# Kernel optimization log

Measured on AMD Instinct MI355X. Metric: run time of the kernel, lower is better.

Reference implementation:

```python
import jax, jax.numpy as jnp
import numpy as np

B, T_ENC, H, L, V = 32, 1024, 1024, 511, 512
SOS = 0


def setup_inputs() -> dict:
    key = jax.random.key(0)
    ks = jax.random.split(key, 16)
    s = 0.02
    inp = {
        "encoder_outputs": jax.random.normal(ks[0], (B, T_ENC, H), jnp.float32),
        "encoder_output_lengths": jnp.clip(
            jax.random.randint(ks[1], (B,), 0, T_ENC), 1, T_ENC
        ).astype(jnp.int64 if jax.config.jax_enable_x64 else jnp.int32),
        "input_labels": jax.random.randint(ks[2], (B, L), 0, V),
        # parameters
        "emb": jax.random.normal(ks[3], (V, H), jnp.float32) * s,
        "lin_in": jax.random.normal(ks[4], (H, H), jnp.float32) * s,      # attention linear_in (no bias)
        "lin_out": jax.random.normal(ks[5], (H, 2 * H), jnp.float32) * s,  # attention linear_out (no bias)
        "gru_w_ih0": jax.random.normal(ks[6], (3 * H, H), jnp.float32) * s,
        "gru_w_hh0": jax.random.normal(ks[7], (3 * H, H), jnp.float32) * s,
        "gru_b_ih0": jax.random.normal(ks[8], (3 * H,), jnp.float32) * s,
        "gru_b_hh0": jax.random.normal(ks[9], (3 * H,), jnp.float32) * s,
        "gru_w_ih1": jax.random.normal(ks[10], (3 * H, H), jnp.float32) * s,
        "gru_w_hh1": jax.random.normal(ks[11], (3 * H, H), jnp.float32) * s,
        "gru_b_ih1": jax.random.normal(ks[12], (3 * H,), jnp.float32) * s,
        "gru_b_hh1": jax.random.normal(ks[13], (3 * H,), jnp.float32) * s,
        "fc_w": jax.random.normal(ks[14], (V, H), jnp.float32) * s,
        "fc_b": jax.random.normal(ks[15], (V,), jnp.float32) * s,
    }
    return inp


def _gru_layer(x_proj, w_hh, b_hh):
    """x_proj: [B, T, 3H] precomputed input projection (incl. b_ih). Torch gate order r,z,n."""
    h0 = jnp.zeros((x_proj.shape[0], w_hh.shape[1]), x_proj.dtype)

    def step(h, xp):
        gh = h @ w_hh.T + b_hh
        xr, xz, xn = jnp.split(xp, 3, axis=-1)
        hr, hz, hn = jnp.split(gh, 3, axis=-1)
        r = jax.nn.sigmoid(xr + hr)
        z = jax.nn.sigmoid(xz + hz)
        n = jnp.tanh(xn + r * hn)
        h_new = (1.0 - z) * n + z * h
        return h_new, h_new

    _, ys = jax.lax.scan(step, h0, x_proj.transpose(1, 0, 2))
    return ys.transpose(1, 0, 2)  # [B, T, H]


def reference(encoder_outputs, encoder_output_lengths, input_labels, emb,
              lin_in, lin_out, gru_w_ih0, gru_w_hh0, gru_b_ih0, gru_b_hh0,
              gru_w_ih1, gru_w_hh1, gru_b_ih1, gru_b_hh1, fc_w, fc_b):
    Bsz = encoder_outputs.shape[0]
    # prepend SOS token (teacher forcing path)
    labels = jnp.concatenate(
        [jnp.full((Bsz, 1), SOS, dtype=input_labels.dtype), input_labels], axis=1
    )  # [B, L+1]
    x = emb[labels]  # [B, L+1, H] (dropout p=0 -> identity)

    # Attention (type='general')
    q = jnp.einsum("bqd,ed->bqe", x, lin_in)  # linear_in(query)
    scores = jnp.einsum("bqd,bkd->bqk", q, encoder_outputs)  # [B, L+1, T]
    t = encoder_outputs.shape[1]
    mask = jnp.arange(t)[None, :] >= encoder_output_lengths[:, None]  # [B, T]
    scores = jnp.where(mask[:, None, :], -jnp.inf, scores)
    w = jax.nn.softmax(scores, axis=-1)
    mix = jnp.einsum("bqk,bkd->bqd", w, encoder_outputs)
    combined = jnp.concatenate([mix, q], axis=-1)  # [B, L+1, 2H]
    attn_out = jnp.tanh(jnp.einsum("bqc,dc->bqd", combined, lin_out))

    # 2-layer GRU (rnn2)
    xp0 = jnp.einsum("btd,gd->btg", attn_out, gru_w_ih0) + gru_b_ih0
    y0 = _gru_layer(xp0, gru_w_hh0, gru_b_hh0)
    xp1 = jnp.einsum("btd,gd->btg", y0, gru_w_ih1) + gru_b_ih1
    y1 = _gru_layer(xp1, gru_w_hh1, gru_b_hh1)

    logits = jnp.einsum("btd,vd->btv", y1, fc_w) + fc_b
    return jax.nn.log_softmax(logits, axis=-1)  # [B, L+1, V]
```

## Files before the change

kernel.cpp:

```cpp
#include <hip/hip_runtime.h>

typedef unsigned short u16;
typedef unsigned int u32;
typedef short bs8 __attribute__((ext_vector_type(8)));
typedef float f4_t __attribute__((ext_vector_type(4)));

#define NB   32
#define TSEQ 512
#define TENC 1024
#define HD   1024
#define VOC  512
#define FS   32
#define POLL_CAP (1 << 22)

#define AS1 __attribute__((address_space(1)))
#define AS3 __attribute__((address_space(3)))

__device__ __forceinline__ float b2f(u16 u) {
  union { u32 i; float f; } x; x.i = ((u32)u) << 16; return x.f;
}
__device__ __forceinline__ u16 f2b(float f) {
  union { float ff; u32 i; } x; x.ff = f;
  u32 r = x.i + 0x7fff + ((x.i >> 16) & 1);
  return (u16)(r >> 16);
}
__device__ __forceinline__ float inF(const void* p, size_t i, int bf) {
  return bf ? b2f(((const u16*)p)[i]) : ((const float*)p)[i];
}
__device__ __forceinline__ void inF4(const void* p, size_t i, int bf, float* o) {
  if (bf) {
    ushort4 u = *reinterpret_cast<const ushort4*>((const u16*)p + i);
    o[0] = b2f(u.x); o[1] = b2f(u.y); o[2] = b2f(u.z); o[3] = b2f(u.w);
  } else {
    float4 v = *reinterpret_cast<const float4*>((const float*)p + i);
    o[0] = v.x; o[1] = v.y; o[2] = v.z; o[3] = v.w;
  }
}
__device__ __forceinline__ void outF(void* p, size_t i, float v, int bf) {
  if (bf) ((u16*)p)[i] = f2b(v);
  else ((float*)p)[i] = v;
}
__device__ __forceinline__ void gld16(const void* g, void* l) {
  __builtin_amdgcn_global_load_lds((const AS1 u32*)g, (AS3 u32*)l, 16, 0, 0);
}
__device__ __forceinline__ u32 aLoad(u32* p) {
  return __hip_atomic_load(p, __ATOMIC_RELAXED, __HIP_MEMORY_SCOPE_AGENT);
}
__device__ __forceinline__ void aStore(u32* p, u32 v) {
  __hip_atomic_store(p, v, __ATOMIC_RELAXED, __HIP_MEMORY_SCOPE_AGENT);
}
__device__ __forceinline__ uint4 ldUC(const char* p) {
  uint4 r;
  asm volatile("global_load_dwordx4 %0, %1, off sc0 sc1" : "=v"(r) : "v"(p));
  return r;
}
__device__ __forceinline__ void stUCshort(char* p, u32 v) {
  asm volatile("global_store_short %0, %1, off sc0 sc1" :: "v"(p), "v"(v) : "memory");
}
__device__ __forceinline__ void waitVM0() {
  asm volatile("s_waitcnt vmcnt(0)" ::: "memory");
}

__global__ void k_detect(const u32* __restrict__ w, int* __restrict__ flag) {
  __shared__ int cnt;
  if (threadIdx.x == 0) cnt = 0;
  __syncthreads();
  int c = 0;
  for (int i = threadIdx.x; i < 1024; i += 256) {
    u32 e = (w[i] >> 7) & 0xFF;
    if (e >= 100 && e <= 126) c++;
  }
  atomicAdd(&cnt, c);
  __syncthreads();
  if (threadIdx.x == 0) flag[0] = (cnt >= 512) ? 1 : 0;
}

__global__ __launch_bounds__(256) void k_f2bf(
    const void* __restrict__ in, u16* __restrict__ out, const int* __restrict__ flagp) {
  const int bf = flagp[0];
  size_t i = ((size_t)blockIdx.x * 256 + threadIdx.x) * 4;
  float v[4]; inF4(in, i, bf, v);
  ushort4 o; o.x = f2b(v[0]); o.y = f2b(v[1]); o.z = f2b(v[2]); o.w = f2b(v[3]);
  *reinterpret_cast<ushort4*>(&out[i]) = o;
}

__global__ __launch_bounds__(256) void k_embed(
    const int* __restrict__ labels, const void* __restrict__ emb,
    u16* __restrict__ x, const int* __restrict__ flagp) {
  const int bf = flagp[0];
  const int m = blockIdx.x;
  const int b = m >> 9, t = m & 511;
  const int lab = (t == 0) ? 0 : labels[b * 511 + t - 1];
  const size_t src = (size_t)lab * HD;
  const size_t dst = (size_t)m * HD;
  const int k = threadIdx.x * 4;
  float v[4]; inF4(emb, src + k, bf, v);
  ushort4 o; o.x = f2b(v[0]); o.y = f2b(v[1]); o.z = f2b(v[2]); o.w = f2b(v[3]);
  *reinterpret_cast<ushort4*>(&x[dst + k]) = o;
}

__global__ __launch_bounds__(256) void k_transpose(
    const void* __restrict__ enc, u16* __restrict__ encT, const int* __restrict__ flagp) {
  const int bf = flagp[0];
  __shared__ float tile[32][33];
  const int b = blockIdx.z, t0 = blockIdx.x * 32, h0 = blockIdx.y * 32;
  const int i = threadIdx.x >> 5, j = threadIdx.x & 31;
  const size_t base = (size_t)b * (TENC * HD);
#pragma unroll
  for (int rr = 0; rr < 4; rr++) {
    int r = i + rr * 8;
    tile[r][j] = inF(enc, base + (size_t)(t0 + r) * HD + h0 + j, bf);
  }
  __syncthreads();
#pragma unroll
  for (int rr = 0; rr < 4; rr++) {
    int r = i + rr * 8;
    encT[base + (size_t)(h0 + r) * TENC + t0 + j] = f2b(tile[j][r]);
  }
}

__global__ __launch_bounds__(256) void k_mfma_gemm(
    const u16* __restrict__ A, const u16* __restrict__ Bm, int K, int lda, int ldb,
    long strideA, long strideB, long strideC,
    void* __restrict__ C, int ldc, int cmode, int act,
    const void* __restrict__ bias, const int* __restrict__ flagp) {
  const int bf = flagp[0];
  __shared__ u16 lsA[8192];
  __shared__ u16 lsB[8192];
  const int tid = threadIdx.x;
  const int l = tid & 63, w = tid >> 6;
  const int wr = w >> 1, wc = w & 1;
  const long m0 = (long)blockIdx.x * 128;
  const long n0 = (long)blockIdx.y * 128;
  const long bz = blockIdx.z;
  const u16* Ab = A + bz * strideA;
  const u16* Bb = Bm + bz * strideB;

  f4_t acc[4][4] = {};
  const int srow = w * 8 + (l >> 3);
  const int schx = (l & 7) * 16;

  for (int kt = 0; kt < K; kt += 64) {
#pragma unroll
    for (int i = 0; i < 4; i++) {
      const int row = i * 32 + srow;
      const char* ga = (const char*)(Ab + (m0 + row) * (long)lda + kt)
                       + (schx ^ ((row & 7) << 4));
      gld16(ga, (char*)lsA + i * 4096 + w * 1024);
    }
#pragma unroll
    for (int i = 0; i < 4; i++) {
      const int row = i * 32 + srow;
      const char* gb = (const char*)(Bb + (n0 + row) * (long)ldb + kt)
                       + (schx ^ ((row & 7) << 4));
      gld16(gb, (char*)lsB + i * 4096 + w * 1024);
    }
    __syncthreads();
#pragma unroll
    for (int h = 0; h < 2; h++) {
      bs8 af[4], bfr[4];
#pragma unroll
      for (int i = 0; i < 4; i++) {
        const int row = wr * 64 + i * 16 + (l & 15);
        const int byt = row * 128 + (((h * 64) + ((l >> 4) * 16)) ^ ((row & 7) << 4));
        af[i] = *(const bs8*)((const char*)lsA + byt);
      }
#pragma unroll
      for (int j = 0; j < 4; j++) {
        const int row = wc * 64 + j * 16 + (l & 15);
        const int byt = row * 128 + (((h * 64) + ((l >> 4) * 16)) ^ ((row & 7) << 4));
        bfr[j] = *(const bs8*)((const char*)lsB + byt);
      }
#pragma unroll
      for (int i = 0; i < 4; i++)
#pragma unroll
        for (int j = 0; j < 4; j++)
          acc[i][j] = __builtin_amdgcn_mfma_f32_16x16x32_bf16(af[i], bfr[j], acc[i][j], 0, 0, 0);
    }
    __syncthreads();
  }

  float bv[4] = {0.f, 0.f, 0.f, 0.f};
  if (bias) {
#pragma unroll
    for (int j = 0; j < 4; j++)
      bv[j] = inF(bias, (size_t)(n0 + wc * 64 + j * 16 + (l & 15)), bf);
  }
#pragma unroll
  for (int i = 0; i < 4; i++) {
#pragma unroll
    for (int j = 0; j < 4; j++) {
      const long rowb = m0 + wr * 64 + i * 16 + ((l >> 4) * 4);
      const long col = n0 + wc * 64 + j * 16 + (l & 15);
#pragma unroll
      for (int r = 0; r < 4; r++) {
        float v = acc[i][j][r] + bv[j];
        if (act == 1) v = tanhf(v);
        const long row = rowb + r;
        if (cmode == 0) {
          ((u16*)C)[bz * strideC + row * (long)ldc + col] = f2b(v);
        } else if (cmode == 1) {
          ((float*)C)[bz * strideC + row * (long)ldc + col] = v;
        } else {
          ((u16*)C)[((long)(row & 511) * 32 + (row >> 9)) * (long)ldc + col] = f2b(v);
        }
      }
    }
  }
}

__global__ __launch_bounds__(256) void k_softmax(
    u16* __restrict__ S, const int* __restrict__ lens) {
  const int m = blockIdx.x;
  const int b = m >> 9;
  const int len = lens[b];
  const int tid = threadIdx.x;
  const size_t base = (size_t)m * TENC;
  float v[4];
  float mx = -1e30f;
#pragma unroll
  for (int i = 0; i < 4; i++) {
    int j = tid + i * 256;
    float s = b2f(S[base + j]);
    v[i] = (j < len) ? s : -1e30f;
    mx = fmaxf(mx, v[i]);
  }
  __shared__ float red[8];
  for (int o = 32; o; o >>= 1) mx = fmaxf(mx, __shfl_xor(mx, o, 64));
  if ((tid & 63) == 0) red[tid >> 6] = mx;
  __syncthreads();
  mx = fmaxf(fmaxf(red[0], red[1]), fmaxf(red[2], red[3]));
  float e[4]; float sum = 0.f;
#pragma unroll
  for (int i = 0; i < 4; i++) {
    e[i] = (v[i] > -1e29f) ? expf(v[i] - mx) : 0.f;
    sum += e[i];
  }
  for (int o = 32; o; o >>= 1) sum += __shfl_xor(sum, o, 64);
  __shared__ float red2[8];
  if ((tid & 63) == 0) red2[tid >> 6] = sum;
  __syncthreads();
  sum = red2[0] + red2[1] + red2[2] + red2[3];
  const float inv = 1.f / sum;
#pragma unroll
  for (int i = 0; i < 4; i++) S[base + tid + i * 256] = f2b(e[i] * inv);
}

__global__ __launch_bounds__(256) void k_packw(
    const void* __restrict__ Wih, const void* __restrict__ Whh,
    u16* __restrict__ out, int fused, const int* __restrict__ flagp) {
  const int bf = flagp[0];
  const long idx = (long)blockIdx.x * 256 + threadIdx.x;
  const int l = (int)(idx & 63);
  int ks, c16, blk;
  if (fused) { ks = (int)((idx >> 6) & 63); c16 = (int)((idx >> 12) & 1); blk = (int)(idx >> 13); }
  else       { ks = (int)((idx >> 6) & 31); c16 = (int)((idx >> 11) & 1); blk = (int)(idx >> 12); }
  const int v = blk * 32 + c16 * 16 + (l & 15);
  const int f = v >> 2, slot = v & 3;
  const int k = ks * 32 + ((l >> 4) << 3);
  const void* W = Whh; long row = 0; bool zero = false; int kk = k;
  if (!fused) {
    if (slot == 0) row = f;
    else if (slot == 1) row = 1024 + f;
    else if (slot == 2) row = 2048 + f;
    else zero = true;
  } else {
    const bool xp = (k < 1024); kk = k & 1023;
    W = xp ? Wih : Whh;
    if (slot == 0) row = f;
    else if (slot == 1) row = 1024 + f;
    else if (slot == 2) { row = 2048 + f; zero = !xp; }
    else { row = 2048 + f; zero = xp; }
  }
  u16 o[8];
#pragma unroll
  for (int e = 0; e < 8; e++)
    o[e] = zero ? (u16)0 : f2b(inF(W, (size_t)row * 1024 + kk + e, bf));
  ushort4* dst = (ushort4*)(out + idx * 8);
  dst[0] = make_ushort4(o[0], o[1], o[2], o[3]);
  dst[1] = make_ushort4(o[4], o[5], o[6], o[7]);
}

__device__ __forceinline__ void stage64(const char* src, char* dst, int tid) {
#pragma unroll
  for (int bh = 0; bh < 2; bh++) {
    uint4 v[8];
#pragma unroll
    for (int i = 0; i < 8; i++)
      v[i] = ldUC(src + (bh * 8 + i) * 4096 + tid * 16);
    waitVM0();
#pragma unroll
    for (int i = 0; i < 8; i++)
      *(uint4*)(dst + (bh * 8 + i) * 4096 + tid * 16) = v[i];
  }
}
__device__ __forceinline__ void waitpair(u32* flags, int aL0, int aL1, int tid) {
  if (tid < 64) {
    int guard = 0;
    while (1) {
      const int v0 = (int)aLoad(flags + (size_t)tid * FS);
      const int v1 = (int)aLoad(flags + (size_t)(tid + 64) * FS);
      const int v2 = (int)aLoad(flags + (size_t)(tid + 128) * FS);
      const int v3 = (int)aLoad(flags + (size_t)(tid + 192) * FS);
      const bool ok = (v0 >= aL0) && (v1 >= aL0) && (v2 >= aL1) && (v3 >= aL1);
      if (__all(ok)) break;
      if (++guard > POLL_CAP) break;
      __builtin_amdgcn_s_sleep(1);
    }
  }
  __syncthreads();
}

__global__ void __launch_bounds__(256, 1) k_gru_p(
    const u16* __restrict__ xp0, const u16* __restrict__ wpk0, const u16* __restrict__ wpk1,
    const void* __restrict__ bhh0, const void* __restrict__ bih1, const void* __restrict__ bhh1,
    u16* __restrict__ y1, char* h0buf, char* h1buf, u32* flags,
    const int* __restrict__ flagp) {
  extern __shared__ char smem[];
  float* red = (float*)(smem + 131072);
  const int bf = flagp[0];
  const int tid = threadIdx.x, l = tid & 63, w = tid >> 6;
  const int nh = w & 1, kh = w >> 1;
  const int g = blockIdx.x;
  const bool isL0 = (g < 128);
  const int gg = isL0 ? g : g - 128;
  const int fl = (l & 15) >> 2;
  const int F = gg * 8 + nh * 4 + fl;
  const int bl0 = (l & 48) | (fl << 2);

  float hprev[2][4] = {{0.f, 0.f, 0.f, 0.f}, {0.f, 0.f, 0.f, 0.f}};

  if (isL0) {
    const u16* W = wpk0 + (size_t)gg * 32768;
    const float br = inF(bhh0, (size_t)F, bf);
    const float bz = inF(bhh0, (size_t)(1024 + F), bf);
    const float bn = inF(bhh0, (size_t)(2048 + F), bf);
    for (int t = 0; t < TSEQ; t++) {
      waitpair(flags, t, t - 1, tid);
      stage64(h0buf + (t & 1) * 65536, smem, tid);
      __syncthreads();
      f4_t S[2] = {};
#pragma unroll 4
      for (int ksl = 0; ksl < 16; ksl++) {
        const int ks = kh * 16 + ksl;
        const bs8 bb = *(const bs8*)(W + (((size_t)(nh * 32 + ks) * 64 + l) << 3));
#pragma unroll
        for (int mt = 0; mt < 2; mt++) {
          const int row = mt * 16 + (l & 15);
          const int byt = row * 2048 + ((ks * 64 + ((l >> 4) << 4)) ^ ((row & 7) << 4));
          const bs8 aa = *(const bs8*)(smem + byt);
          S[mt] = __builtin_amdgcn_mfma_f32_16x16x32_bf16(aa, bb, S[mt], 0, 0, 0);
        }
      }
      if (kh == 1) {
#pragma unroll
        for (int mt = 0; mt < 2; mt++)
          *(f4_t*)&red[((nh * 2 + mt) * 64 + l) * 4] = S[mt];
      }
      __syncthreads();
      if (kh == 0) {
#pragma unroll
        for (int mt = 0; mt < 2; mt++)
          S[mt] += *(const f4_t*)&red[((nh * 2 + mt) * 64 + l) * 4];
        char* hw = h0buf + ((t + 1) & 1) * 65536;
#pragma unroll
        for (int mt = 0; mt < 2; mt++) {
#pragma unroll
          for (int r = 0; r < 4; r++) {
            const int b = mt * 16 + ((l >> 4) << 2) + r;
            const float hr = __shfl(S[mt][r], bl0);
            const float hz = __shfl(S[mt][r], bl0 + 1);
            const float hn = __shfl(S[mt][r], bl0 + 2);
            const long xb = (long)t * 98304 + (long)b * 3072 + F;
            const float xr = b2f(xp0[xb]);
            const float xz = b2f(xp0[xb + 1024]);
            const float xn = b2f(xp0[xb + 2048]);
            const float rr = 1.f / (1.f + expf(-(xr + hr + br)));
            const float zz = 1.f / (1.f + expf(-(xz + hz + bz)));
            const float nn = tanhf(xn + rr * (hn + bn));
            const float hv = (1.f - zz) * nn + zz * hprev[mt][r];
            hprev[mt][r] = hv;
            if ((l & 3) == 0) {
              const int swb = b * 2048 + ((2 * F) ^ ((b & 7) << 4));
              stUCshort(hw + swb, (u32)f2b(hv));
            }
          }
        }
      }
      waitVM0();
      __syncthreads();
      if (tid == 0) aStore(flags + (size_t)g * FS, (u32)(t + 1));
    }
  } else {
    const u16* W = wpk1 + (size_t)gg * 65536;
    const float br = inF(bih1, (size_t)F, bf) + inF(bhh1, (size_t)F, bf);
    const float bz = inF(bih1, (size_t)(1024 + F), bf) + inF(bhh1, (size_t)(1024 + F), bf);
    const float bxn = inF(bih1, (size_t)(2048 + F), bf);
    const float bhn = inF(bhh1, (size_t)(2048 + F), bf);
    for (int s = 0; s < TSEQ; s++) {
      waitpair(flags, s + 1, s, tid);
      stage64(h0buf + ((s + 1) & 1) * 65536, smem, tid);
      stage64(h1buf + (s & 1) * 65536, smem + 65536, tid);
      __syncthreads();
      f4_t S[2] = {};
#pragma unroll 4
      for (int ksl = 0; ksl < 32; ksl++) {
        const int ks = kh * 32 + ksl;
        const bs8 bb = *(const bs8*)(W + (((size_t)(nh * 64 + ks) * 64 + l) << 3));
        const int base = (ks >= 32) ? 65536 : 0;
        const int ks5 = ks & 31;
#pragma unroll
        for (int mt = 0; mt < 2; mt++) {
          const int row = mt * 16 + (l & 15);
          const int byt = base + row * 2048 + ((ks5 * 64 + ((l >> 4) << 4)) ^ ((row & 7) << 4));
          const bs8 aa = *(const bs8*)(smem + byt);
          S[mt] = __builtin_amdgcn_mfma_f32_16x16x32_bf16(aa, bb, S[mt], 0, 0, 0);
        }
      }
      if (kh == 1) {
#pragma unroll
        for (int mt = 0; mt < 2; mt++)
          *(f4_t*)&red[((nh * 2 + mt) * 64 + l) * 4] = S[mt];
      }
      __syncthreads();
      if (kh == 0) {
#pragma unroll
        for (int mt = 0; mt < 2; mt++)
          S[mt] += *(const f4_t*)&red[((nh * 2 + mt) * 64 + l) * 4];
        char* hw = h1buf + ((s + 1) & 1) * 65536;
#pragma unroll
        for (int mt = 0; mt < 2; mt++) {
#pragma unroll
          for (int r = 0; r < 4; r++) {
            const int b = mt * 16 + ((l >> 4) << 2) + r;
            const float rs = __shfl(S[mt][r], bl0);
            const float zs = __shfl(S[mt][r], bl0 + 1);
            const float xnp = __shfl(S[mt][r], bl0 + 2);
            const float hnp = __shfl(S[mt][r], bl0 + 3);
            const float rr = 1.f / (1.f + expf(-(rs + br)));
            const float zz = 1.f / (1.f + expf(-(zs + bz)));
            const float nn = tanhf((xnp + bxn) + rr * (hnp + bhn));
            const float hv = (1.f - zz) * nn + zz * hprev[mt][r];
            hprev[mt][r] = hv;
            if ((l & 3) == 0) {
              const int swb = b * 2048 + ((2 * F) ^ ((b & 7) << 4));
              stUCshort(hw + swb, (u32)f2b(hv));
              y1[((long)b * 512 + s) * 1024 + F] = f2b(hv);
            }
          }
        }
      }
      waitVM0();
      __syncthreads();
      if (tid == 0) aStore(flags + (size_t)g * FS, (u32)(s + 1));
    }
  }
}

__global__ __launch_bounds__(256) void k_logsoftmax(
    const float* __restrict__ L, void* __restrict__ out, const int* __restrict__ flagp) {
  const int bf = flagp[0];
  const int m = blockIdx.x;
  const int tid = threadIdx.x;
  const size_t base = (size_t)m * VOC;
  float v0 = L[base + tid], v1 = L[base + tid + 256];
  float mx = fmaxf(v0, v1);
  __shared__ float red[8];
  for (int o = 32; o; o >>= 1) mx = fmaxf(mx, __shfl_xor(mx, o, 64));
  if ((tid & 63) == 0) red[tid >> 6] = mx;
  __syncthreads();
  mx = fmaxf(fmaxf(red[0], red[1]), fmaxf(red[2], red[3]));
  float s = expf(v0 - mx) + expf(v1 - mx);
  for (int o = 32; o; o >>= 1) s += __shfl_xor(s, o, 64);
  __shared__ float red2[8];
  if ((tid & 63) == 0) red2[tid >> 6] = s;
  __syncthreads();
  s = red2[0] + red2[1] + red2[2] + red2[3];
  const float lse = mx + logf(s);
  outF(out, base + tid, v0 - lse, bf);
  outF(out, base + tid + 256, v1 - lse, bf);
}

extern "C" void kernel_launch(void* const* d_in, const int* in_sizes, int n_in,
                              void* d_out, int out_size, void* d_ws, size_t ws_size,
                              hipStream_t stream) {
  const void* enc = d_in[0];
  const int* lens = (const int*)d_in[1];
  const int* labels = (const int*)d_in[2];
  const void* emb = d_in[3];
  const void* lin_in = d_in[4];
  const void* lin_out = d_in[5];
  const void* w_ih0 = d_in[6];
  const void* w_hh0 = d_in[7];
  const void* b_ih0 = d_in[8];
  const void* b_hh0 = d_in[9];
  const void* w_ih1 = d_in[10];
  const void* w_hh1 = d_in[11];
  const void* b_ih1 = d_in[12];
  const void* b_hh1 = d_in[13];
  const void* fc_w = d_in[14];
  const void* fc_b = d_in[15];

  char* ws = (char*)d_ws;
  const size_t SZ = (size_t)NB * TSEQ * HD * 2;
  int* flag = (int*)ws;
  u16* R0 = (u16*)(ws + 256);
  u16* R1 = (u16*)(ws + 256 + SZ);
  u16* R2 = (u16*)(ws + 256 + 2 * SZ);
  char* R4 = ws + 256 + 4 * SZ;

  char* R2u = (char*)R2 + SZ;
  u16* wpk0 = (u16*)R2u;
  u16* wpk1 = (u16*)(R2u + 8388608);
  char* hreg = R2u + 25165824;
  u32* flagsbuf = (u32*)hreg;
  char* h0buf = hreg + 32768;
  char* h1buf = hreg + 32768 + 131072;
  const size_t hreg_bytes = 32768 + 262144;

  u16* scores = (u16*)R4;
  u16* wli = (u16*)(R4 + 35651584);
  u16* wlo = (u16*)(R4 + 37748736);
  u16* xp0 = (u16*)R4;
  u16* wfc = (u16*)R4;
  float* logits = (float*)(R4 + 1048576);

  k_detect<<<1, 256, 0, stream>>>((const u32*)emb, flag);
  k_embed<<<NB * TSEQ, 256, 0, stream>>>(labels, emb, R0, flag);
  k_f2bf<<<32768, 256, 0, stream>>>(enc, R1, flag);
  k_f2bf<<<1024, 256, 0, stream>>>(lin_in, wli, flag);
  k_f2bf<<<2048, 256, 0, stream>>>(lin_out, wlo, flag);

  k_mfma_gemm<<<dim3(128, 8, 1), 256, 0, stream>>>(
      R0, wli, HD, HD, HD, 0, 0, 0, (void*)(R2 + 1024), 2 * HD, 0, 0, nullptr, flag);
  k_transpose<<<dim3(32, 32, NB), 256, 0, stream>>>(enc, R0, flag);
  k_mfma_gemm<<<dim3(4, 8, NB), 256, 0, stream>>>(
      R2 + 1024, R1, HD, 2 * HD, HD,
      (long)TSEQ * 2 * HD, (long)TENC * HD, (long)TSEQ * TENC,
      (void*)scores, TENC, 0, 0, nullptr, flag);
  k_softmax<<<NB * TSEQ, 256, 0, stream>>>(scores, lens);
  k_mfma_gemm<<<dim3(4, 8, NB), 256, 0, stream>>>(
      scores, R0, TENC, TENC, TENC,
      (long)TSEQ * TENC, (long)HD * TENC, (long)TSEQ * 2 * HD,
      (void*)R2, 2 * HD, 0, 0, nullptr, flag);
  k_mfma_gemm<<<dim3(128, 8, 1), 256, 0, stream>>>(
      R2, wlo, 2 * HD, 2 * HD, 2 * HD, 0, 0, 0,
      (void*)R0, HD, 0, 1, nullptr, flag);

  k_packw<<<2048, 256, 0, stream>>>(nullptr, w_hh0, wpk0, 0, flag);
  k_packw<<<4096, 256, 0, stream>>>(w_ih1, w_hh1, wpk1, 1, flag);
  k_f2bf<<<3072, 256, 0, stream>>>(w_ih0, R1, flag);
  k_mfma_gemm<<<dim3(128, 24, 1), 256, 0, stream>>>(
      R0, R1, HD, HD, HD, 0, 0, 0, (void*)xp0, 3 * HD, 2, 0, b_ih0, flag);

  hipMemsetAsync(hreg, 0, hreg_bytes, stream);
  hipFuncSetAttribute((const void*)k_gru_p,
                      hipFuncAttributeMaxDynamicSharedMemorySize, 139264);
  u16* y1p = R2;
  void* args[] = {&xp0, &wpk0, &wpk1,
                  (void*)&b_hh0, (void*)&b_ih1, (void*)&b_hh1,
                  &y1p, &h0buf, &h1buf, &flagsbuf, &flag};
  hipLaunchCooperativeKernel((const void*)k_gru_p, dim3(256), dim3(256),
                             args, 139264, stream);

  k_f2bf<<<512, 256, 0, stream>>>(fc_w, wfc, flag);
  k_mfma_gemm<<<dim3(128, 4, 1), 256, 0, stream>>>(
      R2, wfc, HD, HD, HD, 0, 0, 0, (void*)logits, VOC, 1, 0, fc_b, flag);
  k_logsoftmax<<<NB * TSEQ, 256, 0, stream>>>(logits, d_out, flag);
}
```

Before: 5.830 ms.

## Fuse both GRU layers into one wavefront loop on half the blocks

The persistent GRU kernel used to give layer 0 and layer 1 their own 128 blocks, each waiting on a pair of flag sets. Now 128 blocks each compute layer 0 at step tau and layer 1 at step tau-1 in the same iteration. A single all-block flag barrier per iteration replaces the pairwise waits. This halves the number of barrier participants and flag polls per step, but each block now does both matmuls serially, so per-step compute on the critical path goes up.

```diff
diff --git a/kernel.cpp b/kernel.cpp
--- a/kernel.cpp
+++ b/kernel.cpp
@@ -294,15 +294,13 @@
       *(uint4*)(dst + (bh * 8 + i) * 4096 + tid * 16) = v[i];
   }
 }
-__device__ __forceinline__ void waitpair(u32* flags, int aL0, int aL1, int tid) {
-  if (tid < 64) {
+__device__ __forceinline__ void waitall(u32* flags, int target, int tid) {
+  if (target > 0 && tid < 64) {
     int guard = 0;
     while (1) {
       const int v0 = (int)aLoad(flags + (size_t)tid * FS);
       const int v1 = (int)aLoad(flags + (size_t)(tid + 64) * FS);
-      const int v2 = (int)aLoad(flags + (size_t)(tid + 128) * FS);
-      const int v3 = (int)aLoad(flags + (size_t)(tid + 192) * FS);
-      const bool ok = (v0 >= aL0) && (v1 >= aL0) && (v2 >= aL1) && (v3 >= aL1);
+      const bool ok = (v0 >= target) && (v1 >= target);
       if (__all(ok)) break;
       if (++guard > POLL_CAP) break;
       __builtin_amdgcn_s_sleep(1);
@@ -317,69 +315,98 @@
     u16* __restrict__ y1, char* h0buf, char* h1buf, u32* flags,
     const int* __restrict__ flagp) {
   extern __shared__ char smem[];
-  float* red = (float*)(smem + 131072);
+  float* red0 = (float*)(smem + 131072);
+  float* red1 = (float*)(smem + 135168);
   const int bf = flagp[0];
   const int tid = threadIdx.x, l = tid & 63, w = tid >> 6;
   const int nh = w & 1, kh = w >> 1;
   const int g = blockIdx.x;
-  const bool isL0 = (g < 128);
-  const int gg = isL0 ? g : g - 128;
   const int fl = (l & 15) >> 2;
-  const int F = gg * 8 + nh * 4 + fl;
+  const int F = g * 8 + nh * 4 + fl;
   const int bl0 = (l & 48) | (fl << 2);
-
-  float hprev[2][4] = {{0.f, 0.f, 0.f, 0.f}, {0.f, 0.f, 0.f, 0.f}};
-
-  if (isL0) {
-    const u16* W = wpk0 + (size_t)gg * 32768;
-    const float br = inF(bhh0, (size_t)F, bf);
-    const float bz = inF(bhh0, (size_t)(1024 + F), bf);
-    const float bn = inF(bhh0, (size_t)(2048 + F), bf);
-    for (int t = 0; t < TSEQ; t++) {
-      waitpair(flags, t, t - 1, tid);
-      stage64(h0buf + (t & 1) * 65536, smem, tid);
-      __syncthreads();
-      f4_t S[2] = {};
+  const char* W0 = (const char*)(wpk0 + (size_t)g * 32768);
+  const char* W1 = (const char*)(wpk1 + (size_t)g * 65536);
+
+  const float b0r = inF(bhh0, (size_t)F, bf);
+  const float b0z = inF(bhh0, (size_t)(1024 + F), bf);
+  const float b0n = inF(bhh0, (size_t)(2048 + F), bf);
+  const float b1r = inF(bih1, (size_t)F, bf) + inF(bhh1, (size_t)F, bf);
+  const float b1z = inF(bih1, (size_t)(1024 + F), bf) + inF(bhh1, (size_t)(1024 + F), bf);
+  const float b1xn = inF(bih1, (size_t)(2048 + F), bf);
+  const float b1hn = inF(bhh1, (size_t)(2048 + F), bf);
+
+  float h0prev[2][4] = {{0.f, 0.f, 0.f, 0.f}, {0.f, 0.f, 0.f, 0.f}};
+  float h1prev[2][4] = {{0.f, 0.f, 0.f, 0.f}, {0.f, 0.f, 0.f, 0.f}};
+
+  for (int tau = 0; tau <= 512; tau++) {
+    waitall(flags, tau, tid);
+    stage64(h0buf + (tau & 1) * 65536, smem, tid);
+    if (tau >= 1) stage64(h1buf + ((tau - 1) & 1) * 65536, smem + 65536, tid);
+    __syncthreads();
+
+    f4_t S0[2] = {}, S1[2] = {};
+    if (tau < 512) {
 #pragma unroll 4
       for (int ksl = 0; ksl < 16; ksl++) {
         const int ks = kh * 16 + ksl;
-        const bs8 bb = *(const bs8*)(W + (((size_t)(nh * 32 + ks) * 64 + l) << 3));
+        const bs8 bb = *(const bs8*)(W0 + (((size_t)(nh * 32 + ks) * 64 + l) << 4));
 #pragma unroll
         for (int mt = 0; mt < 2; mt++) {
           const int row = mt * 16 + (l & 15);
           const int byt = row * 2048 + ((ks * 64 + ((l >> 4) << 4)) ^ ((row & 7) << 4));
           const bs8 aa = *(const bs8*)(smem + byt);
-          S[mt] = __builtin_amdgcn_mfma_f32_16x16x32_bf16(aa, bb, S[mt], 0, 0, 0);
+          S0[mt] = __builtin_amdgcn_mfma_f32_16x16x32_bf16(aa, bb, S0[mt], 0, 0, 0);
         }
       }
-      if (kh == 1) {
+    }
+    if (tau >= 1) {
+#pragma unroll 4
+      for (int ksl = 0; ksl < 32; ksl++) {
+        const int ks = kh * 32 + ksl;
+        const bs8 bb = *(const bs8*)(W1 + (((size_t)(nh * 64 + ks) * 64 + l) << 4));
+        const int base = (ks >= 32) ? 65536 : 0;
+        const int ks5 = ks & 31;
+#pragma unroll
+        for (int mt = 0; mt < 2; mt++) {
+          const int row = mt * 16 + (l & 15);
+          const int byt = base + row * 2048 + ((ks5 * 64 + ((l >> 4) << 4)) ^ ((row & 7) << 4));
+          const bs8 aa = *(const bs8*)(smem + byt);
+          S1[mt] = __builtin_amdgcn_mfma_f32_16x16x32_bf16(aa, bb, S1[mt], 0, 0, 0);
+        }
+      }
+    }
+    if (kh == 1) {
+#pragma unroll
+      for (int mt = 0; mt < 2; mt++) {
+        *(f4_t*)&red0[((nh * 2 + mt) * 64 + l) * 4] = S0[mt];
+        *(f4_t*)&red1[((nh * 2 + mt) * 64 + l) * 4] = S1[mt];
+      }
+    }
+    __syncthreads();
+    if (kh == 0) {
+      if (tau < 512) {
+        const int t = tau;
 #pragma unroll
         for (int mt = 0; mt < 2; mt++)
-          *(f4_t*)&red[((nh * 2 + mt) * 64 + l) * 4] = S[mt];
-      }
-      __syncthreads();
-      if (kh == 0) {
-#pragma unroll
-        for (int mt = 0; mt < 2; mt++)
-          S[mt] += *(const f4_t*)&red[((nh * 2 + mt) * 64 + l) * 4];
-        char* hw = h0buf + ((t + 1) & 1) * 65536;
+          S0[mt] += *(const f4_t*)&red0[((nh * 2 + mt) * 64 + l) * 4];
+        char* hw = h0buf + ((tau + 1) & 1) * 65536;
 #pragma unroll
         for (int mt = 0; mt < 2; mt++) {
 #pragma unroll
           for (int r = 0; r < 4; r++) {
             const int b = mt * 16 + ((l >> 4) << 2) + r;
-            const float hr = __shfl(S[mt][r], bl0);
-            const float hz = __shfl(S[mt][r], bl0 + 1);
-            const float hn = __shfl(S[mt][r], bl0 + 2);
+            const float hr = __shfl(S0[mt][r], bl0);
+            const float hz = __shfl(S0[mt][r], bl0 + 1);
+            const float hn = __shfl(S0[mt][r], bl0 + 2);
             const long xb = (long)t * 98304 + (long)b * 3072 + F;
             const float xr = b2f(xp0[xb]);
             const float xz = b2f(xp0[xb + 1024]);
             const float xn = b2f(xp0[xb + 2048]);
-            const float rr = 1.f / (1.f + expf(-(xr + hr + br)));
-            const float zz = 1.f / (1.f + expf(-(xz + hz + bz)));
-            const float nn = tanhf(xn + rr * (hn + bn));
-            const float hv = (1.f - zz) * nn + zz * hprev[mt][r];
-            hprev[mt][r] = hv;
+            const float rr = 1.f / (1.f + expf(-(xr + hr + b0r)));
+            const float zz = 1.f / (1.f + expf(-(xz + hz + b0z)));
+            const float nn = tanhf(xn + rr * (hn + b0n));
+            const float hv = (1.f - zz) * nn + zz * h0prev[mt][r];
+            h0prev[mt][r] = hv;
             if ((l & 3) == 0) {
               const int swb = b * 2048 + ((2 * F) ^ ((b & 7) << 4));
               stUCshort(hw + swb, (u32)f2b(hv));
@@ -387,61 +414,26 @@
           }
         }
       }
-      waitVM0();
-      __syncthreads();
-      if (tid == 0) aStore(flags + (size_t)g * FS, (u32)(t + 1));
-    }
-  } else {
-    const u16* W = wpk1 + (size_t)gg * 65536;
-    const float br = inF(bih1, (size_t)F, bf) + inF(bhh1, (size_t)F, bf);
-    const float bz = inF(bih1, (size_t)(1024 + F), bf) + inF(bhh1, (size_t)(1024 + F), bf);
-    const float bxn = inF(bih1, (size_t)(2048 + F), bf);
-    const float bhn = inF(bhh1, (size_t)(2048 + F), bf);
-    for (int s = 0; s < TSEQ; s++) {
-      waitpair(flags, s + 1, s, tid);
-      stage64(h0buf + ((s + 1) & 1) * 65536, smem, tid);
-      stage64(h1buf + (s & 1) * 65536, smem + 65536, tid);
-      __syncthreads();
-      f4_t S[2] = {};
-#pragma unroll 4
-      for (int ksl = 0; ksl < 32; ksl++) {
-        const int ks = kh * 32 + ksl;
-        const bs8 bb = *(const bs8*)(W + (((size_t)(nh * 64 + ks) * 64 + l) << 3));
-        const int base = (ks >= 32) ? 65536 : 0;
-        const int ks5 = ks & 31;
-#pragma unroll
-        for (int mt = 0; mt < 2; mt++) {
-          const int row = mt * 16 + (l & 15);
-          const int byt = base + row * 2048 + ((ks5 * 64 + ((l >> 4) << 4)) ^ ((row & 7) << 4));
-          const bs8 aa = *(const bs8*)(smem + byt);
-          S[mt] = __builtin_amdgcn_mfma_f32_16x16x32_bf16(aa, bb, S[mt], 0, 0, 0);
-        }
-      }
-      if (kh == 1) {
+      if (tau >= 1) {
+        const int s = tau - 1;
 #pragma unroll
         for (int mt = 0; mt < 2; mt++)
-          *(f4_t*)&red[((nh * 2 + mt) * 64 + l) * 4] = S[mt];
-      }
-      __syncthreads();
-      if (kh == 0) {
-#pragma unroll
-        for (int mt = 0; mt < 2; mt++)
-          S[mt] += *(const f4_t*)&red[((nh * 2 + mt) * 64 + l) * 4];
-        char* hw = h1buf + ((s + 1) & 1) * 65536;
+          S1[mt] += *(const f4_t*)&red1[((nh * 2 + mt) * 64 + l) * 4];
+        char* hw = h1buf + (tau & 1) * 65536;
 #pragma unroll
         for (int mt = 0; mt < 2; mt++) {
 #pragma unroll
           for (int r = 0; r < 4; r++) {
             const int b = mt * 16 + ((l >> 4) << 2) + r;
-            const float rs = __shfl(S[mt][r], bl0);
-            const float zs = __shfl(S[mt][r], bl0 + 1);
-            const float xnp = __shfl(S[mt][r], bl0 + 2);
-            const float hnp = __shfl(S[mt][r], bl0 + 3);
-            const float rr = 1.f / (1.f + expf(-(rs + br)));
-            const float zz = 1.f / (1.f + expf(-(zs + bz)));
-            const float nn = tanhf((xnp + bxn) + rr * (hnp + bhn));
-            const float hv = (1.f - zz) * nn + zz * hprev[mt][r];
-            hprev[mt][r] = hv;
+            const float rs = __shfl(S1[mt][r], bl0);
+            const float zs = __shfl(S1[mt][r], bl0 + 1);
+            const float xnp = __shfl(S1[mt][r], bl0 + 2);
+            const float hnp = __shfl(S1[mt][r], bl0 + 3);
+            const float rr = 1.f / (1.f + expf(-(rs + b1r)));
+            const float zz = 1.f / (1.f + expf(-(zs + b1z)));
+            const float nn = tanhf((xnp + b1xn) + rr * (hnp + b1hn));
+            const float hv = (1.f - zz) * nn + zz * h1prev[mt][r];
+            h1prev[mt][r] = hv;
             if ((l & 3) == 0) {
               const int swb = b * 2048 + ((2 * F) ^ ((b & 7) << 4));
               stUCshort(hw + swb, (u32)f2b(hv));
@@ -450,10 +442,10 @@
           }
         }
       }
-      waitVM0();
-      __syncthreads();
-      if (tid == 0) aStore(flags + (size_t)g * FS, (u32)(s + 1));
-    }
+    }
+    waitVM0();
+    __syncthreads();
+    if (tid == 0) aStore(flags + (size_t)g * FS, (u32)(tau + 1));
   }
 }
 
@@ -560,7 +552,7 @@
   void* args[] = {&xp0, &wpk0, &wpk1,
                   (void*)&b_hh0, (void*)&b_ih1, (void*)&b_hh1,
                   &y1p, &h0buf, &h1buf, &flagsbuf, &flag};
-  hipLaunchCooperativeKernel((const void*)k_gru_p, dim3(256), dim3(256),
+  hipLaunchCooperativeKernel((const void*)k_gru_p, dim3(128), dim3(256),
                              args, 139264, stream);
 
   k_f2bf<<<512, 256, 0, stream>>>(fc_w, wfc, flag);
```

Measured after the change: 11.06 ms. 1.9x slower.
